# Kernel optimization log

Measured on AMD Instinct MI355X. Metric: run time of the kernel, lower is better.

Reference implementation:

```python
import jax, jax.numpy as jnp
import numpy as np

D_MODEL = 1024
NHEAD = 16
D_K = D_MODEL // NHEAD


def setup_inputs() -> dict:
    key = jax.random.key(0)
    ks = jax.random.split(key, 11)
    B, S = 2, 2048
    scale = 1.0 / np.sqrt(D_MODEL)
    inp = {
        "q": jax.random.normal(ks[0], (B, S, D_MODEL), jnp.float32),
        "k": jax.random.normal(ks[1], (B, S, D_MODEL), jnp.float32),
        "v": jax.random.normal(ks[2], (B, S, D_MODEL), jnp.float32),
        "Wq": jax.random.normal(ks[3], (D_MODEL, D_MODEL), jnp.float32) * scale,
        "bq": jnp.zeros((D_MODEL,), jnp.float32),
        "Wk": jax.random.normal(ks[4], (D_MODEL, D_MODEL), jnp.float32) * scale,
        "bk": jnp.zeros((D_MODEL,), jnp.float32),
        "Wv": jax.random.normal(ks[5], (D_MODEL, D_MODEL), jnp.float32) * scale,
        "bv": jnp.zeros((D_MODEL,), jnp.float32),
        "Wo": jax.random.normal(ks[6], (D_MODEL, D_MODEL), jnp.float32) * scale,
        "bo": jnp.zeros((D_MODEL,), jnp.float32),
    }
    return inp


def reference(q, k, v, Wq, bq, Wk, bk, Wv, bv, Wo, bo):
    B, S, _ = q.shape
    # Linear projections (torch Linear: x @ W.T + b), split into heads
    def proj(x, W, b):
        y = jnp.einsum('bsd,ed->bse', x, W) + b
        return y.reshape(B, -1, NHEAD, D_K).transpose(0, 2, 1, 3)  # [B,H,S,Dk]

    qh = proj(q, Wq, bq)
    kh = proj(k, Wk, bk)
    vh = proj(v, Wv, bv)

    scores = jnp.einsum('bhqd,bhkd->bhqk', qh, kh) / jnp.sqrt(
        jnp.asarray(D_K, qh.dtype))
    attn = jax.nn.softmax(scores, axis=-1)  # dropout is identity in eval
    out = jnp.einsum('bhqk,bhkd->bhqd', attn, vh)
    out = out.transpose(0, 2, 1, 3).reshape(B, S, D_MODEL)
    return jnp.einsum('bsd,ed->bse', out, Wo) + bo
```

## Files before the change

kernel.cpp:

```cpp
#include <hip/hip_runtime.h>
#include <stdint.h>
#include <stddef.h>

#define D_MODEL 1024
#define NHEAD   16
#define DK      64
#define BB      2
#define SS      2048
#define NTOK    (BB*SS)

#define SCALE_Q 0.18033688011f

typedef short  short8 __attribute__((ext_vector_type(8)));
typedef __bf16 bf16x8 __attribute__((ext_vector_type(8)));
typedef float  f32x4  __attribute__((ext_vector_type(4)));

__device__ __forceinline__ unsigned short f2bf(float x){
  unsigned int u = __builtin_bit_cast(unsigned int, x);
  u += 0x7fffu + ((u >> 16) & 1u);
  return (unsigned short)(u >> 16);
}

__device__ __forceinline__ unsigned int pack_bf2(float x, float y){
  unsigned int a = __builtin_bit_cast(unsigned int, x) + 0x8000u;
  unsigned int b = __builtin_bit_cast(unsigned int, y) + 0x8000u;
  return __builtin_amdgcn_perm(b, a, 0x07060302u);
}

__device__ __forceinline__ unsigned int cvt_pk_bf16(float lo, float hi){
  unsigned int r;
  asm("v_cvt_pk_bf16_f32 %0, %1, %2" : "=v"(r) : "v"(lo), "v"(hi));
  return r;
}

__device__ __forceinline__ float fast_exp2(float x){
#if __has_builtin(__builtin_amdgcn_exp2f)
  return __builtin_amdgcn_exp2f(x);
#else
  return exp2f(x);
#endif
}

__device__ __forceinline__ f32x4 mfma16(bf16x8 a, bf16x8 b, f32x4 c){
  return __builtin_amdgcn_mfma_f32_16x16x32_bf16(a, b, c, 0, 0, 0);
}

__device__ __forceinline__ void async16(const void* g, void* lds){
  __builtin_amdgcn_global_load_lds(
      (const __attribute__((address_space(1))) unsigned int*)g,
      (__attribute__((address_space(3))) unsigned int*)lds,
      16, 0, 0);
}

__global__ __launch_bounds__(256) void cast_bf16_all(
    const float* __restrict__ q,  const float* __restrict__ k,  const float* __restrict__ v,
    const float* __restrict__ wq, const float* __restrict__ wk, const float* __restrict__ wv,
    const float* __restrict__ wo,
    unsigned short* __restrict__ qb,  unsigned short* __restrict__ kb,  unsigned short* __restrict__ vb,
    unsigned short* __restrict__ wqb, unsigned short* __restrict__ wkb, unsigned short* __restrict__ wvb,
    unsigned short* __restrict__ wob)
{
  const float* src; unsigned short* dst; int n;
  switch (blockIdx.y){
    case 0: src = q;  dst = qb;  n = NTOK*D_MODEL;    break;
    case 1: src = k;  dst = kb;  n = NTOK*D_MODEL;    break;
    case 2: src = v;  dst = vb;  n = NTOK*D_MODEL;    break;
    case 3: src = wq; dst = wqb; n = D_MODEL*D_MODEL; break;
    case 4: src = wk; dst = wkb; n = D_MODEL*D_MODEL; break;
    case 5: src = wv; dst = wvb; n = D_MODEL*D_MODEL; break;
    default: src = wo; dst = wob; n = D_MODEL*D_MODEL; break;
  }
  int i = (blockIdx.x * 256 + threadIdx.x) * 8;
  if (i >= n) return;
  float4 a = *(const float4*)(src + i);
  float4 b = *(const float4*)(src + i + 4);
  short8 o;
  o[0] = (short)f2bf(a.x); o[1] = (short)f2bf(a.y);
  o[2] = (short)f2bf(a.z); o[3] = (short)f2bf(a.w);
  o[4] = (short)f2bf(b.x); o[5] = (short)f2bf(b.y);
  o[6] = (short)f2bf(b.z); o[7] = (short)f2bf(b.w);
  *(short8*)(dst + i) = o;
}

__global__ __launch_bounds__(256) void qkv_gemm(
    const unsigned short* __restrict__ qb, const unsigned short* __restrict__ kb,
    const unsigned short* __restrict__ vb,
    const unsigned short* __restrict__ wqb, const unsigned short* __restrict__ wkb,
    const unsigned short* __restrict__ wvb,
    const float* __restrict__ bq, const float* __restrict__ bk, const float* __restrict__ bv,
    unsigned short* __restrict__ Qh, unsigned short* __restrict__ Kh, unsigned short* __restrict__ Vt)
{
  __shared__ __align__(16) unsigned short S[128*128];
  unsigned short* As0 = S;
  unsigned short* Bs0 = S + 4096;
  unsigned short* As1 = S + 8192;
  unsigned short* Bs1 = S + 12288;

  int bid = blockIdx.x;
  const int id = (bid & 7) * 96 + (bid >> 3);
  const int z = id >> 8, r = id & 255;
  const unsigned short *A, *Bt; const float* bias; unsigned short* C;
  int bm, bn, N, brow; float scale;
  if (z == 0){ A = qb;  Bt = wqb; bias = bq; C = Qh; bm = (r>>3)*128; bn = (r&7)*128; N = 1024; brow = 0; scale = SCALE_Q; }
  else if (z == 1){ A = kb;  Bt = wkb; bias = bk; C = Kh; bm = (r>>3)*128; bn = (r&7)*128; N = 1024; brow = 0; scale = 1.0f; }
  else            { A = wvb; Bt = vb;  bias = bv; C = Vt; bm = (r&7)*128; bn = (r>>3)*128; N = 4096; brow = 1; scale = 1.0f; }
  const int K = 1024;
  const int tid  = threadIdx.x, lane = tid & 63, w = tid >> 6;
  const int quad = lane >> 4,   l16  = lane & 15;
  const int wm = w >> 1, wn = w & 1;
  const int fsl = (quad ^ ((l16 >> 2) & 3)) << 3;

  const unsigned short* asrc[2];
  const unsigned short* bsrc[2];
  #pragma unroll
  for (int c = 0; c < 2; ++c){
    int s = (w*2 + c)*64 + lane;
    int row = s >> 2, c4 = s & 3;
    int cs = (c4 ^ ((row >> 2) & 3)) << 3;
    asrc[c] = A  + (size_t)(bm + row)*K + cs;
    bsrc[c] = Bt + (size_t)(bn + row)*K + cs;
  }

  #pragma unroll
  for (int c = 0; c < 2; ++c){
    async16(asrc[c], (char*)As0 + (w*2 + c)*1024);
    async16(bsrc[c], (char*)Bs0 + (w*2 + c)*1024);
    asrc[c] += 32; bsrc[c] += 32;
  }

  f32x4 acc[4][4] = {};
  for (int t = 0; t < 32; ++t){
    const int cur = t & 1;
    unsigned short* An = cur ? As0 : As1;
    unsigned short* Bn = cur ? Bs0 : Bs1;
    #pragma unroll
    for (int c = 0; c < 2; ++c){
      async16(asrc[c], (char*)An + (w*2 + c)*1024);
      async16(bsrc[c], (char*)Bn + (w*2 + c)*1024);
      asrc[c] += 32; bsrc[c] += 32;
    }
    asm volatile("s_waitcnt vmcnt(4)\n\ts_barrier" ::: "memory");

    const unsigned short* Ac = cur ? As1 : As0;
    const unsigned short* Bc = cur ? Bs1 : Bs0;
    bf16x8 af[4], bf[4];
    #pragma unroll
    for (int mt = 0; mt < 4; ++mt){
      af[mt] = *(const bf16x8*)&Ac[(wm*64 + mt*16 + l16)*32 + fsl];
      bf[mt] = *(const bf16x8*)&Bc[(wn*64 + mt*16 + l16)*32 + fsl];
    }
    #pragma unroll
    for (int mt = 0; mt < 4; ++mt)
      #pragma unroll
      for (int nt = 0; nt < 4; ++nt)
        acc[mt][nt] = mfma16(bf[nt], af[mt], acc[mt][nt]);

    asm volatile("s_waitcnt lgkmcnt(0)\n\ts_barrier" ::: "memory");
  }
  asm volatile("s_waitcnt vmcnt(0)\n\ts_barrier" ::: "memory");

  #pragma unroll
  for (int nt = 0; nt < 4; ++nt){
    int nl = wn*64 + nt*16 + 4*quad;
    float4 b4;
    if (!brow) b4 = *(const float4*)&bias[bn + nl];
    #pragma unroll
    for (int mt = 0; mt < 4; ++mt){
      int ml = wm*64 + mt*16 + l16;
      float bmv = brow ? bias[bm + ml] : 0.0f;
      float v0 = (acc[mt][nt][0] + (brow ? bmv : b4.x)) * scale;
      float v1 = (acc[mt][nt][1] + (brow ? bmv : b4.y)) * scale;
      float v2 = (acc[mt][nt][2] + (brow ? bmv : b4.z)) * scale;
      float v3 = (acc[mt][nt][3] + (brow ? bmv : b4.w)) * scale;
      uint2 p; p.x = pack_bf2(v0, v1); p.y = pack_bf2(v2, v3);
      int gl = nl >> 2;
      if (brow){
        int g3 = gl & 7;
        gl = (gl & ~7) | ((g3 & 3)*2 + (g3 >> 2));
      }
      int gs = gl ^ (ml & 14);
      *(uint2*)&S[ml*128 + gs*4] = p;
    }
  }
  __syncthreads();
  {
    int rr_ = tid >> 1, hf = tid & 1;
    size_t rowbase = (size_t)(bm + rr_) * N + bn;
    #pragma unroll
    for (int i = 0; i < 8; ++i){
      int gg = hf*16 + i*2;
      uint4 d = *(const uint4*)&S[rr_*128 + ((gg ^ (rr_ & 14)) << 2)];
      *(uint4*)&C[rowbase + gg*4] = d;
    }
  }
}

__global__ __launch_bounds__(256) void gemm_out(
    const unsigned short* __restrict__ A, const unsigned short* __restrict__ Bt,
    const float* __restrict__ bias, float* __restrict__ C)
{
  __shared__ __align__(16) unsigned short As[64*64];
  __shared__ __align__(16) unsigned short Bs[128*64];
  const int K = 1024, N = 1024;
  const int tid  = threadIdx.x, lane = tid & 63, w = tid >> 6;
  const int quad = lane >> 4,   l16  = lane & 15;
  const int bm = blockIdx.y * 64, bn = blockIdx.x * 128;
  const int sw = l16 & 7;
  f32x4 acc[4][2] = {};
  for (int kb_ = 0; kb_ < 16; ++kb_){
    const int k0 = kb_ << 6;
    __syncthreads();
    #pragma unroll
    for (int c = 0; c < 2; ++c){
      int chunk = (w*2 + c)*64 + lane;
      int row = chunk >> 3, c8 = chunk & 7;
      async16(A + (size_t)(bm + row)*K + k0 + ((c8 ^ (row & 7)) << 3),
              (char*)As + (w*2 + c)*1024);
    }
    #pragma unroll
    for (int c = 0; c < 4; ++c){
      int chunk = (w*4 + c)*64 + lane;
      int row = chunk >> 3, c8 = chunk & 7;
      async16(Bt + (size_t)(bn + row)*K + k0 + ((c8 ^ (row & 7)) << 3),
              (char*)Bs + (w*4 + c)*1024);
    }
    __syncthreads();
    bf16x8 af[4][2], bf[2][2];
    #pragma unroll
    for (int mt = 0; mt < 4; ++mt)
      #pragma unroll
      for (int ks = 0; ks < 2; ++ks)
        af[mt][ks] = *(const bf16x8*)&As[(mt*16 + l16)*64 + (((ks*4 + quad) ^ sw) << 3)];
    #pragma unroll
    for (int nt = 0; nt < 2; ++nt)
      #pragma unroll
      for (int ks = 0; ks < 2; ++ks)
        bf[nt][ks] = *(const bf16x8*)&Bs[(w*32 + nt*16 + l16)*64 + (((ks*4 + quad) ^ sw) << 3)];
    #pragma unroll
    for (int ks = 0; ks < 2; ++ks)
      #pragma unroll
      for (int mt = 0; mt < 4; ++mt)
        #pragma unroll
        for (int nt = 0; nt < 2; ++nt)
          acc[mt][nt] = mfma16(af[mt][ks], bf[nt][ks], acc[mt][nt]);
  }
  #pragma unroll
  for (int mt = 0; mt < 4; ++mt){
    #pragma unroll
    for (int nt = 0; nt < 2; ++nt){
      int col = bn + w*32 + nt*16 + l16;
      float bc = bias[col];
      #pragma unroll
      for (int rr = 0; rr < 4; ++rr){
        int row = bm + mt*16 + quad*4 + rr;
        C[(size_t)row*N + col] = acc[mt][nt][rr] + bc;
      }
    }
  }
}

__global__ __launch_bounds__(256) void attn(
    const unsigned short* __restrict__ Qh, const unsigned short* __restrict__ Kh,
    const unsigned short* __restrict__ Vt, unsigned short* __restrict__ ctx)
{
  __shared__ __align__(16) unsigned short Kbuf[2][64*64];
  __shared__ __align__(16) unsigned short Vbuf[2][64*64];
  __shared__ __align__(16) unsigned short QP[128*64];

  const int tid  = threadIdx.x, lane = tid & 63, w = tid >> 6;
  const int quad = lane >> 4,   l16  = lane & 15;
  const int b = blockIdx.y >> 4, h = blockIdx.y & 15;
  const int q0 = blockIdx.x * 128;
  const int sw = l16 & 7;

  #pragma unroll
  for (int c = 0; c < 4; ++c){
    int s = (w*4 + c)*64 + lane;
    int row = s >> 3, c8 = s & 7;
    async16(Qh + (size_t)(b*SS + q0 + row)*D_MODEL + h*DK + ((c8 ^ (row & 7)) << 3),
            (char*)QP + (w*4 + c)*1024);
  }

  const unsigned short* Kp = Kh + (size_t)(b*SS)*D_MODEL + h*DK;
  const unsigned short* Vp = Vt + (size_t)(h*DK)*NTOK + b*SS;
  const unsigned short* ksrc[2];
  const unsigned short* vsrc[2];
  #pragma unroll
  for (int c = 0; c < 2; ++c){
    int s = (w*2 + c)*64 + lane;
    int row = s >> 3, c8 = s & 7;
    int cs = (c8 ^ (row & 7)) << 3;
    ksrc[c] = Kp + (size_t)row*D_MODEL + cs;
    vsrc[c] = Vp + (size_t)row*NTOK  + cs;
  }

  #pragma unroll
  for (int c = 0; c < 2; ++c){
    async16(ksrc[c], (char*)Kbuf[0] + (w*2 + c)*1024);
    async16(vsrc[c], (char*)Vbuf[0] + (w*2 + c)*1024);
    ksrc[c] += 64*D_MODEL;
    vsrc[c] += 64;
  }
  __syncthreads();

  bf16x8 bq0[2], bq1[2];
  #pragma unroll
  for (int ks = 0; ks < 2; ++ks){
    bq0[ks] = *(const bf16x8*)&QP[(w*32 +      l16)*64 + (((ks*4 + quad) ^ sw) << 3)];
    bq1[ks] = *(const bf16x8*)&QP[(w*32 + 16 + l16)*64 + (((ks*4 + quad) ^ sw) << 3)];
  }

  f32x4 acc[2][4] = {};
  float l0a = 0.0f, l0b = 0.0f, l1a = 0.0f, l1b = 0.0f;

  for (int it = 0; it < 32; ++it){
    const int cur = it & 1;
    #pragma unroll
    for (int c = 0; c < 2; ++c){
      async16(ksrc[c], (char*)Kbuf[1 - cur] + (w*2 + c)*1024);
      async16(vsrc[c], (char*)Vbuf[1 - cur] + (w*2 + c)*1024);
      ksrc[c] += 64*D_MODEL;
      vsrc[c] += 64;
    }
    asm volatile("s_waitcnt vmcnt(4)\n\ts_barrier" ::: "memory");

    const unsigned short* Kc = Kbuf[cur];
    const unsigned short* Vc = Vbuf[cur];

    bf16x8 kf[4][2];
    #pragma unroll
    for (int mt = 0; mt < 4; ++mt)
      #pragma unroll
      for (int ks = 0; ks < 2; ++ks)
        kf[mt][ks] = *(const bf16x8*)&Kc[(mt*16 + l16)*64 + (((ks*4 + quad) ^ sw) << 3)];

    bf16x8 vf[4][2];
    #pragma unroll
    for (int nt = 0; nt < 4; ++nt)
      #pragma unroll
      for (int ks = 0; ks < 2; ++ks)
        vf[nt][ks] = *(const bf16x8*)&Vc[(nt*16 + l16)*64 + (((ks*4 + quad) ^ sw) << 3)];

    f32x4 s0[4] = {}, s1[4] = {};
    #pragma unroll
    for (int mt = 0; mt < 4; ++mt)
      #pragma unroll
      for (int ks = 0; ks < 2; ++ks){
        s0[mt] = mfma16(kf[mt][ks], bq0[ks], s0[mt]);
        s1[mt] = mfma16(kf[mt][ks], bq1[ks], s1[mt]);
      }

    float s0a = 0.0f, s0b = 0.0f, s1a = 0.0f, s1b = 0.0f;
    #pragma unroll
    for (int mt = 0; mt < 4; ++mt)
      #pragma unroll
      for (int rr = 0; rr < 4; ++rr){
        float p0 = fast_exp2(s0[mt][rr]); s0[mt][rr] = p0;
        float p1 = fast_exp2(s1[mt][rr]); s1[mt][rr] = p1;
        if (mt & 1){ s0b += p0; s1b += p1; } else { s0a += p0; s1a += p1; }
      }
    l0a += s0a; l0b += s0b; l1a += s1a; l1b += s1b;

    bf16x8 bp0[2], bp1[2];
    #pragma unroll
    for (int ks = 0; ks < 2; ++ks){
      uint4 t;
      t.x = cvt_pk_bf16(s0[2*ks  ][0], s0[2*ks  ][1]);
      t.y = cvt_pk_bf16(s0[2*ks  ][2], s0[2*ks  ][3]);
      t.z = cvt_pk_bf16(s0[2*ks+1][0], s0[2*ks+1][1]);
      t.w = cvt_pk_bf16(s0[2*ks+1][2], s0[2*ks+1][3]);
      bp0[ks] = __builtin_bit_cast(bf16x8, t);
      t.x = cvt_pk_bf16(s1[2*ks  ][0], s1[2*ks  ][1]);
      t.y = cvt_pk_bf16(s1[2*ks  ][2], s1[2*ks  ][3]);
      t.z = cvt_pk_bf16(s1[2*ks+1][0], s1[2*ks+1][1]);
      t.w = cvt_pk_bf16(s1[2*ks+1][2], s1[2*ks+1][3]);
      bp1[ks] = __builtin_bit_cast(bf16x8, t);
    }

    #pragma unroll
    for (int nt = 0; nt < 4; ++nt)
      #pragma unroll
      for (int ks = 0; ks < 2; ++ks){
        acc[0][nt] = mfma16(vf[nt][ks], bp0[ks], acc[0][nt]);
        acc[1][nt] = mfma16(vf[nt][ks], bp1[ks], acc[1][nt]);
      }

    asm volatile("s_waitcnt lgkmcnt(0)\n\ts_barrier" ::: "memory");
  }

  float l_i[2] = { l0a + l0b, l1a + l1b };
  float inv[2];
  #pragma unroll
  for (int qg = 0; qg < 2; ++qg){
    float t = l_i[qg];
    t += __shfl_xor(t, 16);
    t += __shfl_xor(t, 32);
    inv[qg] = 1.0f / t;
  }
  #pragma unroll
  for (int qg = 0; qg < 2; ++qg){
    int pr = (w*32 + qg*16 + l16)*64;
    #pragma unroll
    for (int nt = 0; nt < 4; ++nt){
      int c8  = nt*2 + (quad >> 1);
      int off = ((c8 ^ sw) << 3) + (quad & 1)*4;
      uint2 p;
      p.x = pack_bf2(acc[qg][nt][0]*inv[qg], acc[qg][nt][1]*inv[qg]);
      p.y = pack_bf2(acc[qg][nt][2]*inv[qg], acc[qg][nt][3]*inv[qg]);
      *(uint2*)&QP[pr + off] = p;
    }
  }
  asm volatile("s_waitcnt lgkmcnt(0)" ::: "memory");
  {
    int r  = w*32 + (lane >> 1);
    int j0 = (lane & 1)*4;
    unsigned short* dst = ctx + (size_t)(b*SS + q0 + r)*D_MODEL + h*DK;
    #pragma unroll
    for (int i = 0; i < 4; ++i){
      int j = j0 + i;
      uint4 d = *(const uint4*)&QP[r*64 + ((j ^ (r & 7)) << 3)];
      *(uint4*)(dst + j*8) = d;
    }
  }
}

extern "C" void kernel_launch(void* const* d_in, const int* in_sizes, int n_in,
                              void* d_out, int out_size, void* d_ws, size_t ws_size,
                              hipStream_t stream) {
  const float* q  = (const float*)d_in[0];
  const float* k  = (const float*)d_in[1];
  const float* v  = (const float*)d_in[2];
  const float* Wq = (const float*)d_in[3];
  const float* bq = (const float*)d_in[4];
  const float* Wk = (const float*)d_in[5];
  const float* bk = (const float*)d_in[6];
  const float* Wv = (const float*)d_in[7];
  const float* bv = (const float*)d_in[8];
  const float* Wo = (const float*)d_in[9];
  const float* bo = (const float*)d_in[10];

  char* ws = (char*)d_ws;
  const size_t TOKB = (size_t)NTOK * D_MODEL * 2;
  const size_t WB   = (size_t)D_MODEL * D_MODEL * 2;
  unsigned short* qb  = (unsigned short*)ws;             ws += TOKB;
  unsigned short* kb  = (unsigned short*)ws;             ws += TOKB;
  unsigned short* vb  = (unsigned short*)ws;             ws += TOKB;
  unsigned short* wqb = (unsigned short*)ws;             ws += WB;
  unsigned short* wkb = (unsigned short*)ws;             ws += WB;
  unsigned short* wvb = (unsigned short*)ws;             ws += WB;
  unsigned short* wob = (unsigned short*)ws;             ws += WB;
  unsigned short* Qh  = (unsigned short*)ws;             ws += TOKB;
  unsigned short* Kh  = (unsigned short*)ws;             ws += TOKB;
  unsigned short* Vt  = (unsigned short*)ws;             ws += TOKB;
  unsigned short* ctx = (unsigned short*)ws;             ws += TOKB;

  cast_bf16_all<<<dim3(2048, 7), 256, 0, stream>>>(q, k, v, Wq, Wk, Wv, Wo,
                                                   qb, kb, vb, wqb, wkb, wvb, wob);
  qkv_gemm<<<dim3(768), 256, 0, stream>>>(qb, kb, vb, wqb, wkb, wvb,
                                          bq, bk, bv, Qh, Kh, Vt);
  attn<<<dim3(SS/128, BB*NHEAD), 256, 0, stream>>>(Qh, Kh, Vt, ctx);
  gemm_out<<<dim3(8, 64), 256, 0, stream>>>(ctx, wob, bo, (float*)d_out);
}
```

Baseline: 220.4 us.

## Double-buffer gemm_out LDS tiles and remap blocks for XCD locality

```diff
diff --git a/kernel.cpp b/kernel.cpp
--- a/kernel.cpp
+++ b/kernel.cpp
@@ -199,43 +199,62 @@
     const unsigned short* __restrict__ A, const unsigned short* __restrict__ Bt,
     const float* __restrict__ bias, float* __restrict__ C)
 {
-  __shared__ __align__(16) unsigned short As[64*64];
-  __shared__ __align__(16) unsigned short Bs[128*64];
+  __shared__ __align__(16) unsigned short As[2][64*64];
+  __shared__ __align__(16) unsigned short Bs[2][128*64];
   const int K = 1024, N = 1024;
   const int tid  = threadIdx.x, lane = tid & 63, w = tid >> 6;
   const int quad = lane >> 4,   l16  = lane & 15;
-  const int bm = blockIdx.y * 64, bn = blockIdx.x * 128;
+  int bid = blockIdx.x;
+  const int id = (bid & 7) * 64 + (bid >> 3);
+  const int bm = (id >> 3) * 64, bn = (id & 7) * 128;
   const int sw = l16 & 7;
+
+  const unsigned short* asrc[2];
+  const unsigned short* bsrc[4];
+  #pragma unroll
+  for (int c = 0; c < 2; ++c){
+    int chunk = (w*2 + c)*64 + lane;
+    int row = chunk >> 3, c8 = chunk & 7;
+    asrc[c] = A + (size_t)(bm + row)*K + ((c8 ^ (row & 7)) << 3);
+  }
+  #pragma unroll
+  for (int c = 0; c < 4; ++c){
+    int chunk = (w*4 + c)*64 + lane;
+    int row = chunk >> 3, c8 = chunk & 7;
+    bsrc[c] = Bt + (size_t)(bn + row)*K + ((c8 ^ (row & 7)) << 3);
+  }
+
+  #pragma unroll
+  for (int c = 0; c < 2; ++c){ async16(asrc[c], (char*)As[0] + (w*2 + c)*1024); asrc[c] += 64; }
+  #pragma unroll
+  for (int c = 0; c < 4; ++c){ async16(bsrc[c], (char*)Bs[0] + (w*4 + c)*1024); bsrc[c] += 64; }
+
   f32x4 acc[4][2] = {};
-  for (int kb_ = 0; kb_ < 16; ++kb_){
-    const int k0 = kb_ << 6;
-    __syncthreads();
+  for (int t = 0; t < 16; ++t){
+    const int cur = t & 1;
     #pragma unroll
     for (int c = 0; c < 2; ++c){
-      int chunk = (w*2 + c)*64 + lane;
-      int row = chunk >> 3, c8 = chunk & 7;
-      async16(A + (size_t)(bm + row)*K + k0 + ((c8 ^ (row & 7)) << 3),
-              (char*)As + (w*2 + c)*1024);
+      async16(asrc[c], (char*)As[1 - cur] + (w*2 + c)*1024); asrc[c] += 64;
     }
     #pragma unroll
     for (int c = 0; c < 4; ++c){
-      int chunk = (w*4 + c)*64 + lane;
-      int row = chunk >> 3, c8 = chunk & 7;
-      async16(Bt + (size_t)(bn + row)*K + k0 + ((c8 ^ (row & 7)) << 3),
-              (char*)Bs + (w*4 + c)*1024);
-    }
-    __syncthreads();
+      async16(bsrc[c], (char*)Bs[1 - cur] + (w*4 + c)*1024); bsrc[c] += 64;
+    }
+    asm volatile("s_waitcnt vmcnt(6)\n\ts_barrier" ::: "memory");
+
+    const unsigned short* Ac = As[cur];
+    const unsigned short* Bc = Bs[cur];
     bf16x8 af[4][2], bf[2][2];
     #pragma unroll
     for (int mt = 0; mt < 4; ++mt)
       #pragma unroll
       for (int ks = 0; ks < 2; ++ks)
-        af[mt][ks] = *(const bf16x8*)&As[(mt*16 + l16)*64 + (((ks*4 + quad) ^ sw) << 3)];
+        af[mt][ks] = *(const bf16x8*)&Ac[(mt*16 + l16)*64 + (((ks*4 + quad) ^ sw) << 3)];
     #pragma unroll
     for (int nt = 0; nt < 2; ++nt)
       #pragma unroll
       for (int ks = 0; ks < 2; ++ks)
-        bf[nt][ks] = *(const bf16x8*)&Bs[(w*32 + nt*16 + l16)*64 + (((ks*4 + quad) ^ sw) << 3)];
+        bf[nt][ks] = *(const bf16x8*)&Bs[cur][(w*32 + nt*16 + l16)*64 + (((ks*4 + quad) ^ sw) << 3)];
     #pragma unroll
     for (int ks = 0; ks < 2; ++ks)
       #pragma unroll
@@ -243,7 +262,10 @@
         #pragma unroll
         for (int nt = 0; nt < 2; ++nt)
           acc[mt][nt] = mfma16(af[mt][ks], bf[nt][ks], acc[mt][nt]);
-  }
+
+    asm volatile("s_waitcnt lgkmcnt(0)\n\ts_barrier" ::: "memory");
+  }
+
   #pragma unroll
   for (int mt = 0; mt < 4; ++mt){
     #pragma unroll
@@ -453,11 +475,12 @@
   unsigned short* Kh  = (unsigned short*)ws;             ws += TOKB;
   unsigned short* Vt  = (unsigned short*)ws;             ws += TOKB;
   unsigned short* ctx = (unsigned short*)ws;             ws += TOKB;
+  ws += 4096;
 
   cast_bf16_all<<<dim3(2048, 7), 256, 0, stream>>>(q, k, v, Wq, Wk, Wv, Wo,
                                                    qb, kb, vb, wqb, wkb, wvb, wob);
   qkv_gemm<<<dim3(768), 256, 0, stream>>>(qb, kb, vb, wqb, wkb, wvb,
                                           bq, bk, bv, Qh, Kh, Vt);
   attn<<<dim3(SS/128, BB*NHEAD), 256, 0, stream>>>(Qh, Kh, Vt, ctx);
-  gemm_out<<<dim3(8, 64), 256, 0, stream>>>(ctx, wob, bo, (float*)d_out);
-}
+  gemm_out<<<dim3(512), 256, 0, stream>>>(ctx, wob, bo, (float*)d_out);
+}
```

Result: no change. 220.0 us (-0.2%).
